# Optimization experiments

Hardware: AMD Instinct MI355X
Metric: run time of the kernel (lower is better)

The kernel has to match this reference:

```python
import jax, jax.numpy as jnp
import numpy as np

D_MODEL = 1024
N_HEADS = 16
HEAD_DIM = 64  # 16*64 = 1024
LATENT = 256   # low-rank KV compression dim
NUM_WHEELS = 4
WHEEL_OUT = 256


def setup_inputs() -> dict:
    key = jax.random.key(0)
    ks = jax.random.split(key, 9)
    S = 2048
    s = lambda fan_in: 1.0 / np.sqrt(fan_in)
    return {
        "sketch_emb": jax.random.normal(ks[0], (S, D_MODEL), dtype=jnp.float32),
        "Wq": jax.random.normal(ks[1], (D_MODEL, N_HEADS * HEAD_DIM), dtype=jnp.float32) * s(D_MODEL),
        "Wdkv": jax.random.normal(ks[2], (D_MODEL, LATENT), dtype=jnp.float32) * s(D_MODEL),
        "Wuk": jax.random.normal(ks[3], (LATENT, N_HEADS * HEAD_DIM), dtype=jnp.float32) * s(LATENT),
        "Wuv": jax.random.normal(ks[4], (LATENT, N_HEADS * HEAD_DIM), dtype=jnp.float32) * s(LATENT),
        "Wo": jax.random.normal(ks[5], (N_HEADS * HEAD_DIM, D_MODEL), dtype=jnp.float32) * s(N_HEADS * HEAD_DIM),
        "wheel_W": jax.random.normal(ks[6], (NUM_WHEELS, D_MODEL, WHEEL_OUT), dtype=jnp.float32) * s(D_MODEL),
        "wheel_b": jax.random.normal(ks[7], (NUM_WHEELS, WHEEL_OUT), dtype=jnp.float32) * 0.01,
    }


def reference(sketch_emb, Wq, Wdkv, Wuk, Wuv, Wo, wheel_W, wheel_b):
    S = sketch_emb.shape[0]
    # Multi-head latent attention: per-head Q, shared low-rank KV latent.
    q = (sketch_emb @ Wq).reshape(S, N_HEADS, HEAD_DIM)          # [S,H,D]
    c_kv = sketch_emb @ Wdkv                                      # [S,L]
    k = (c_kv @ Wuk).reshape(S, N_HEADS, HEAD_DIM)                # [S,H,D]
    v = (c_kv @ Wuv).reshape(S, N_HEADS, HEAD_DIM)                # [S,H,D]
    scale = 1.0 / np.sqrt(HEAD_DIM).astype(np.float32)
    scores = jnp.einsum("qhd,khd->hqk", q, k) * scale             # [H,S,S]
    attn = jax.nn.softmax(scores, axis=-1)
    ctx = jnp.einsum("hqk,khd->qhd", attn, v).reshape(S, N_HEADS * HEAD_DIM)
    body = ctx @ Wo                                               # [S,1024]
    # Wheel projections batched as one einsum, then laid out as concat order
    # cat([body, w0, w1, w2, w3], dim=1)
    wheels = jnp.einsum("sd,wde->swe", body, wheel_W) + wheel_b   # [S,W,256]
    wheels = wheels.reshape(S, NUM_WHEELS * WHEEL_OUT)
    return jnp.concatenate([body, wheels], axis=1)                # [S,2048]
```

## Files before the change

kernel.cpp:

```cpp
#include <hip/hip_runtime.h>
#include <math.h>

#define S_LEN 2048
#define DMODEL 1024
#define NHEADS 16
#define HDIM 64
#define QPITCH 1280

typedef _Float16 f16x8 __attribute__((ext_vector_type(8)));
typedef _Float16 f16x4 __attribute__((ext_vector_type(4)));
typedef float    f32x4 __attribute__((ext_vector_type(4)));

__device__ __forceinline__ void gld_lds16(void* lds, const void* g) {
    __builtin_amdgcn_global_load_lds(
        (__attribute__((address_space(1))) void*)(g),
        (__attribute__((address_space(3))) void*)(lds), 16, 0, 0);
}

__device__ __forceinline__ void gemm_core(
    _Float16* sA, _Float16* sB,
    const _Float16* __restrict__ A, int lda,
    const _Float16* __restrict__ Bt, int ldb,
    int nkt,
    _Float16* __restrict__ Cb, int ldcb, int bmode,
    _Float16* __restrict__ Cb2, int ldcb2,
    int bx, int by)
{
    const int tid  = threadIdx.x;
    const int lane = tid & 63;
    const int w    = tid >> 6;
    const int quad = lane >> 4;
    const int c0   = lane & 15;
    const int m0 = by * 128;
    const int n0 = bx * 128;

    const int srow = lane >> 3;
    const int sc   = lane & 7;
    const _Float16* a_src[4]; const _Float16* b_src[4];
    int dstoff[4];
#pragma unroll
    for (int t = 0; t < 4; t++) {
        const int row = w * 32 + t * 8 + srow;
        const int c = sc ^ (row & 7);
        a_src[t] = A  + (size_t)(m0 + row) * lda + c * 8;
        b_src[t] = Bt + (size_t)(n0 + row) * ldb + c * 8;
        dstoff[t] = (w * 32 + t * 8) * 64;
    }

    const int mw = (w & 1) * 64;
    const int nw = (w >> 1) * 64;
    int arow[4], brow[4];
#pragma unroll
    for (int i = 0; i < 4; i++) {
        arow[i] = mw + i * 16 + c0;
        brow[i] = nw + i * 16 + c0;
    }

    f32x4 acc[4][4];
#pragma unroll
    for (int i = 0; i < 4; i++)
#pragma unroll
        for (int j = 0; j < 4; j++) acc[i][j] = (f32x4){0.f, 0.f, 0.f, 0.f};

    auto stage = [&](int buf) {
#pragma unroll
        for (int t = 0; t < 4; t++) {
            gld_lds16(&sA[buf * 8192 + dstoff[t]], a_src[t]); a_src[t] += 64;
            gld_lds16(&sB[buf * 8192 + dstoff[t]], b_src[t]); b_src[t] += 64;
        }
    };
    auto step = [&](int buf) {
#pragma unroll
        for (int ks = 0; ks < 2; ks++) {
            const int cb = ks * 4 + quad;
            f16x8 af[4], bfv[4];
#pragma unroll
            for (int i = 0; i < 4; i++)
                af[i] = *(const f16x8*)&sA[buf * 8192 + arow[i] * 64 + ((cb ^ (arow[i] & 7)) << 3)];
#pragma unroll
            for (int j = 0; j < 4; j++)
                bfv[j] = *(const f16x8*)&sB[buf * 8192 + brow[j] * 64 + ((cb ^ (brow[j] & 7)) << 3)];
#pragma unroll
            for (int i = 0; i < 4; i++)
#pragma unroll
                for (int j = 0; j < 4; j++)
                    acc[i][j] = __builtin_amdgcn_mfma_f32_16x16x32_f16(af[i], bfv[j], acc[i][j], 0, 0, 0);
        }
    };

    stage(0);
    for (int kt = 0; kt < nkt; kt += 2) {
        __syncthreads();
        stage(1);
        step(0);
        __syncthreads();
        if (kt + 2 < nkt) stage(0);
        step(1);
    }

#pragma unroll
    for (int i = 0; i < 4; i++) {
#pragma unroll
        for (int reg = 0; reg < 4; reg++) {
            const int m = m0 + mw + i * 16 + quad * 4 + reg;
#pragma unroll
            for (int j = 0; j < 4; j++) {
                const int n = n0 + nw + j * 16 + c0;
                _Float16 hv = (_Float16)acc[i][j][reg];
                if (bmode == 0) {
                    Cb[(size_t)m * ldcb + n] = hv;
                } else {
                    if (n < 1024) Cb[(size_t)m * ldcb + n] = hv;
                    else          Cb2[(size_t)(n - 1024) * ldcb2 + m] = hv;
                }
            }
        }
    }
}

__global__ __launch_bounds__(256) void gemm_qcwf(
    const _Float16* __restrict__ WcT, const _Float16* __restrict__ Wo_f16,
    _Float16* __restrict__ BtWheels,
    const _Float16* __restrict__ emb_f16, const _Float16* __restrict__ Wqc_t,
    _Float16* __restrict__ qc_f16)
{
    __shared__ _Float16 sA[2][8192];
    __shared__ _Float16 sB[2][8192];
    int b = blockIdx.x;
    if (b < 64) {
        gemm_core(&sA[0][0], &sB[0][0], WcT, 1024, Wo_f16, 1024, 16,
                  BtWheels, 1024, 0, nullptr, 0, b >> 3, b & 7);
    } else {
        b -= 64;
        gemm_core(&sA[0][0], &sB[0][0], emb_f16, 1024, Wqc_t, 1024, 16,
                  qc_f16, 1280, 0, nullptr, 0, b >> 4, b & 15);
    }
}

__global__ __launch_bounds__(256) void gemm_kv(
    const _Float16* __restrict__ qc_f16, const _Float16* __restrict__ Wukv_t,
    _Float16* __restrict__ k_f16, _Float16* __restrict__ vT_f16)
{
    __shared__ _Float16 sA[2][8192];
    __shared__ _Float16 sB[2][8192];
    const int b = blockIdx.x;
    gemm_core(&sA[0][0], &sB[0][0], qc_f16 + 1024, 1280, Wukv_t, 256, 4,
              k_f16, 1024, 4, vT_f16, 2048, b >> 4, b & 15);
}

__global__ __launch_bounds__(256) void gemm_fin64(
    const _Float16* __restrict__ A,
    const _Float16* __restrict__ Bt,
    float* __restrict__ out,
    const float* __restrict__ bias)
{
    __shared__ _Float16 sA[2][64 * 64];
    __shared__ _Float16 sB[2][128 * 64];

    const int tid  = threadIdx.x;
    const int lane = tid & 63;
    const int w    = tid >> 6;
    const int quad = lane >> 4;
    const int c0   = lane & 15;

    const int flat = blockIdx.x;
    const int xcd  = flat & 7;
    const int wi   = flat >> 3;
    const int by   = (xcd & 3) * 8 + (wi & 7);
    const int bx   = (xcd >> 2) * 8 + (wi >> 3);
    const int m0 = by * 64;
    const int n0 = bx * 128;

    const int srow = lane >> 3;
    const int sc   = lane & 7;
    const _Float16* a_src[2]; int a_dst[2];
#pragma unroll
    for (int t = 0; t < 2; t++) {
        const int row = t * 32 + w * 8 + srow;
        const int c = sc ^ (row & 7);
        a_src[t] = A + (size_t)(m0 + row) * 1024 + c * 8;
        a_dst[t] = (t * 32 + w * 8) * 64;
    }
    const _Float16* b_src[4]; int b_dst[4];
#pragma unroll
    for (int t = 0; t < 4; t++) {
        const int row = t * 32 + w * 8 + srow;
        const int c = sc ^ (row & 7);
        b_src[t] = Bt + (size_t)(n0 + row) * 1024 + c * 8;
        b_dst[t] = (t * 32 + w * 8) * 64;
    }

    const int mw = (w & 1) * 32;
    const int nw = (w >> 1) * 64;
    int arow[2], brow[4];
#pragma unroll
    for (int i = 0; i < 2; i++) arow[i] = mw + i * 16 + c0;
#pragma unroll
    for (int j = 0; j < 4; j++) brow[j] = nw + j * 16 + c0;

    f32x4 acc[2][4];
#pragma unroll
    for (int i = 0; i < 2; i++)
#pragma unroll
        for (int j = 0; j < 4; j++) acc[i][j] = (f32x4){0.f, 0.f, 0.f, 0.f};

    auto stage = [&](int buf) {
#pragma unroll
        for (int t = 0; t < 2; t++) { gld_lds16(&sA[buf][a_dst[t]], a_src[t]); a_src[t] += 64; }
#pragma unroll
        for (int t = 0; t < 4; t++) { gld_lds16(&sB[buf][b_dst[t]], b_src[t]); b_src[t] += 64; }
    };
    auto step = [&](int buf) {
#pragma unroll
        for (int ks = 0; ks < 2; ks++) {
            const int cb = ks * 4 + quad;
            f16x8 af[2], bfv[4];
#pragma unroll
            for (int i = 0; i < 2; i++)
                af[i] = *(const f16x8*)&sA[buf][arow[i] * 64 + ((cb ^ (arow[i] & 7)) << 3)];
#pragma unroll
            for (int j = 0; j < 4; j++)
                bfv[j] = *(const f16x8*)&sB[buf][brow[j] * 64 + ((cb ^ (brow[j] & 7)) << 3)];
#pragma unroll
            for (int i = 0; i < 2; i++)
#pragma unroll
                for (int j = 0; j < 4; j++)
                    acc[i][j] = __builtin_amdgcn_mfma_f32_16x16x32_f16(af[i], bfv[j], acc[i][j], 0, 0, 0);
        }
    };

    stage(0);
    for (int kt = 0; kt < 16; kt += 2) {
        __syncthreads();
        stage(1);
        step(0);
        __syncthreads();
        if (kt + 2 < 16) stage(0);
        step(1);
    }

    float bias_v[4];
#pragma unroll
    for (int j = 0; j < 4; j++) bias_v[j] = bias[n0 + nw + j * 16 + c0];
#pragma unroll
    for (int i = 0; i < 2; i++) {
#pragma unroll
        for (int reg = 0; reg < 4; reg++) {
            const int m = m0 + mw + i * 16 + quad * 4 + reg;
#pragma unroll
            for (int j = 0; j < 4; j++) {
                const int n = n0 + nw + j * 16 + c0;
                out[(size_t)m * 2048 + n] = acc[i][j][reg] + bias_v[j];
            }
        }
    }
}

#define SOFT_M2 8.65617024533378f
#define OTP 68

__global__ __launch_bounds__(256) void attn_mfma_kernel(
    const _Float16* __restrict__ qs,
    const _Float16* __restrict__ kk,
    const _Float16* __restrict__ vT,
    float* __restrict__ Opart,
    float* __restrict__ lpart)
{
    __shared__ _Float16 Ks[2][64 * 64];
    __shared__ _Float16 Vt[2][64 * 64];
    __shared__ float    Ot[4][16 * OTP];

    const int flat = blockIdx.x;
    const int g  = flat & 31;
    const int qb = flat >> 5;
    const int h  = g & 15;
    const int kz = g >> 4;
    const int tid  = threadIdx.x;
    const int lane = tid & 63;
    const int w    = tid >> 6;
    const int quad = lane >> 4;
    const int c0   = lane & 15;

    f16x8 qfrag[2][2];
#pragma unroll
    for (int m = 0; m < 2; m++) {
        const _Float16* qrow = qs + (size_t)(qb * 128 + w * 32 + m * 16 + c0) * QPITCH + h * HDIM;
        qfrag[m][0] = *(const f16x8*)(qrow + quad * 8);
        qfrag[m][1] = *(const f16x8*)(qrow + 32 + quad * 8);
    }

    const int srow = lane >> 3;
    const int sc   = lane & 7;
    const _Float16* k_src[2]; const _Float16* v_src[2];
    int dstoff[2];
#pragma unroll
    for (int t = 0; t < 2; t++) {
        const int row = w * 16 + t * 8 + srow;
        const int c = sc ^ (row & 7);
        k_src[t] = kk + (size_t)(kz * 1024 + row) * DMODEL + h * HDIM + c * 8;
        v_src[t] = vT + (size_t)(h * HDIM + row) * S_LEN + kz * 1024 + c * 8;
        dstoff[t] = (w * 16 + t * 8) * 64;
    }

    f32x4 OfragT[2][4];
#pragma unroll
    for (int m = 0; m < 2; m++)
#pragma unroll
        for (int db = 0; db < 4; db++) OfragT[m][db] = (f32x4){0.f, 0.f, 0.f, 0.f};
    float l_r[2] = {0.f, 0.f};

    auto stage = [&](int buf) {
#pragma unroll
        for (int t = 0; t < 2; t++) {
            gld_lds16(&Ks[buf][dstoff[t]], k_src[t]); k_src[t] += (size_t)64 * DMODEL;
            gld_lds16(&Vt[buf][dstoff[t]], v_src[t]); v_src[t] += 64;
        }
    };

    auto attn_step = [&](int buf) {
        f32x4 sfrag[2][4];
#pragma unroll
        for (int m = 0; m < 2; m++)
#pragma unroll
            for (int nb = 0; nb < 4; nb++) sfrag[m][nb] = (f32x4){0.f, 0.f, 0.f, 0.f};
        __builtin_amdgcn_s_setprio(1);
#pragma unroll
        for (int nb = 0; nb < 4; nb++) {
            const int krow = nb * 16 + c0;
#pragma unroll
            for (int ks = 0; ks < 2; ks++) {
                const int cb = ks * 4 + quad;
                f16x8 kfr = *(const f16x8*)&Ks[buf][krow * 64 + ((cb ^ (c0 & 7)) << 3)];
#pragma unroll
                for (int m = 0; m < 2; m++)
                    sfrag[m][nb] = __builtin_amdgcn_mfma_f32_16x16x32_f16(kfr, qfrag[m][ks], sfrag[m][nb], 0, 0, 0);
            }
        }
        __builtin_amdgcn_s_setprio(0);

        f16x4 pfrag[2][4];
#pragma unroll
        for (int m = 0; m < 2; m++)
#pragma unroll
            for (int kb = 0; kb < 4; kb++) {
                float p0 = __builtin_amdgcn_exp2f(sfrag[m][kb][0] - SOFT_M2);
                float p1 = __builtin_amdgcn_exp2f(sfrag[m][kb][1] - SOFT_M2);
                float p2 = __builtin_amdgcn_exp2f(sfrag[m][kb][2] - SOFT_M2);
                float p3 = __builtin_amdgcn_exp2f(sfrag[m][kb][3] - SOFT_M2);
                l_r[m] += (p0 + p1) + (p2 + p3);
                f16x4 pv;
                pv[0] = (_Float16)p0; pv[1] = (_Float16)p1;
                pv[2] = (_Float16)p2; pv[3] = (_Float16)p3;
                pfrag[m][kb] = pv;
            }

        __builtin_amdgcn_s_setprio(1);
#pragma unroll
        for (int kb = 0; kb < 4; kb++) {
            const int cc = (((kb * 2 + (quad >> 1)) ^ (c0 & 7)) << 3) + (quad & 1) * 4;
#pragma unroll
            for (int db = 0; db < 4; db++) {
                f16x4 vf = *(const f16x4*)&Vt[buf][(db * 16 + c0) * 64 + cc];
#pragma unroll
                for (int m = 0; m < 2; m++)
                    OfragT[m][db] = __builtin_amdgcn_mfma_f32_16x16x16f16(vf, pfrag[m][kb], OfragT[m][db], 0, 0, 0);
            }
        }
        __builtin_amdgcn_s_setprio(0);
    };

    stage(0);
    for (int kt = 0; kt < 16; kt += 2) {
        __syncthreads();
        stage(1);
        attn_step(0);
        __syncthreads();
        if (kt + 2 < 16) stage(0);
        attn_step(1);
    }

#pragma unroll
    for (int m = 0; m < 2; m++) {
        float rs = l_r[m];
        rs += __shfl_xor(rs, 16, 64);
        rs += __shfl_xor(rs, 32, 64);
        if (lane < 16)
            lpart[(size_t)(kz * 16 + h) * 2048 + qb * 128 + w * 32 + m * 16 + c0] = rs;
    }

    float* Otw = &Ot[w][0];
#pragma unroll
    for (int m = 0; m < 2; m++) {
#pragma unroll
        for (int db = 0; db < 4; db++)
            *(f32x4*)&Otw[c0 * OTP + db * 16 + quad * 4] = OfragT[m][db];
        __asm__ __volatile__("s_waitcnt lgkmcnt(0)" ::: "memory");
#pragma unroll
        for (int it = 0; it < 4; it++) {
            const int r = it * 4 + quad;
            f32x4 ov = *(const f32x4*)&Otw[r * OTP + c0 * 4];
            const int row = qb * 128 + w * 32 + m * 16 + r;
            *(f32x4*)&Opart[((size_t)kz * 2048 + row) * 1024 + h * 64 + c0 * 4] = ov;
        }
        __asm__ __volatile__("s_waitcnt lgkmcnt(0)" ::: "memory");
    }
}

__global__ __launch_bounds__(256) void attn_combine_kernel(
    const float* __restrict__ Opart, const float* __restrict__ lpart,
    _Float16* __restrict__ ctx)
{
    const int i = blockIdx.x * 256 + threadIdx.x;
    const int row = i >> 8;
    const int c4  = (i & 255) * 4;
    const int h = c4 >> 6;
    const float l = lpart[(size_t)h * 2048 + row] + lpart[(size_t)(16 + h) * 2048 + row];
    const float inv = 1.0f / l;
    float4 o0 = ((const float4*)(Opart + (size_t)row * 1024))[c4 >> 2];
    float4 o1 = ((const float4*)(Opart + (size_t)(2048 + row) * 1024))[c4 >> 2];
    f16x4 v;
    v[0] = (_Float16)((o0.x + o1.x) * inv);
    v[1] = (_Float16)((o0.y + o1.y) * inv);
    v[2] = (_Float16)((o0.z + o1.z) * inv);
    v[3] = (_Float16)((o0.w + o1.w) * inv);
    *(f16x4*)(ctx + (size_t)row * 1024 + c4) = v;
}

__device__ __forceinline__ void xpose_seg(float (*tile)[33],
    const float* __restrict__ src, _Float16* __restrict__ dst,
    int C, int dpitch, float scale, int bx, int by, int nbase0)
{
    const int r0 = by * 32, c0 = bx * 32;
    const int tr = threadIdx.x >> 5, tc = threadIdx.x & 31;
#pragma unroll
    for (int i = 0; i < 4; i++)
        tile[tr + i * 8][tc] = src[(size_t)(r0 + tr + i * 8) * C + c0 + tc];
    __syncthreads();
    const int nr = threadIdx.x & 31;
    const int k0 = (threadIdx.x >> 5) * 4;
    f16x4 hv;
#pragma unroll
    for (int e = 0; e < 4; e++)
        hv[e] = (_Float16)(tile[k0 + e][nr] * scale);
    *(f16x4*)(dst + (size_t)(nbase0 + c0 + nr) * dpitch + (r0 + k0)) = hv;
}

__global__ __launch_bounds__(256) void megaprep_kernel(
    const float* __restrict__ emb, const float* __restrict__ Wq,
    const float* __restrict__ Wdkv, const float* __restrict__ Wuk,
    const float* __restrict__ Wuv, const float* __restrict__ Wo,
    const float* __restrict__ wheelW, const float* __restrict__ wheelB,
    _Float16* __restrict__ Wqc_t, _Float16* __restrict__ Wukv_t,
    _Float16* __restrict__ Bt_full, _Float16* __restrict__ WcT,
    _Float16* __restrict__ Wo_f16, _Float16* __restrict__ emb_f16,
    float* __restrict__ biasbuf)
{
    __shared__ float tile[32][33];
    int b = blockIdx.x;
    const int tid = threadIdx.x;

    if (b < 1024) { xpose_seg(tile, Wq, Wqc_t, 1024, 1024, 0.125f, b & 31, b >> 5, 0); return; }
    b -= 1024;
    if (b < 256)  { xpose_seg(tile, Wdkv, Wqc_t + 1048576, 256, 1024, 1.f, b & 7, b >> 3, 0); return; }
    b -= 256;
    if (b < 256)  { xpose_seg(tile, Wuk, Wukv_t, 1024, 256, 1.4426950408889634f, b & 31, b >> 5, 0); return; }
    b -= 256;
    if (b < 256)  { xpose_seg(tile, Wuv, Wukv_t + 262144, 1024, 256, 1.f, b & 31, b >> 5, 0); return; }
    b -= 256;
    if (b < 1024) { xpose_seg(tile, Wo, Bt_full, 1024, 1024, 1.f, b & 31, b >> 5, 0); return; }
    b -= 1024;
    if (b < 1024) {
        const int z = b >> 8, rem = b & 255;
        xpose_seg(tile, wheelW + (size_t)z * 262144, WcT, 256, 1024, 1.f,
                  rem & 7, rem >> 3, z * 256);
        return;
    }
    b -= 1024;
    if (b < 1024) {
        const int i = b * 256 + tid;
        float4 f = ((const float4*)Wo)[i];
        f16x4 v;
        v[0] = (_Float16)f.x; v[1] = (_Float16)f.y;
        v[2] = (_Float16)f.z; v[3] = (_Float16)f.w;
        ((f16x4*)Wo_f16)[i] = v;
        return;
    }
    b -= 1024;
    if (b < 2048) {
        const int i = b * 256 + tid;
        float4 f = ((const float4*)emb)[i];
        f16x4 v;
        v[0] = (_Float16)f.x; v[1] = (_Float16)f.y;
        v[2] = (_Float16)f.z; v[3] = (_Float16)f.w;
        ((f16x4*)emb_f16)[i] = v;
        return;
    }
    b -= 2048;
    if (b < 8) {
        const int i = b * 256 + tid;
        biasbuf[i] = (i < 1024) ? 0.f : wheelB[i - 1024];
    }
}

extern "C" void kernel_launch(void* const* d_in, const int* in_sizes, int n_in,
                              void* d_out, int out_size, void* d_ws, size_t ws_size,
                              hipStream_t stream) {
    const float* emb    = (const float*)d_in[0];
    const float* Wq     = (const float*)d_in[1];
    const float* Wdkv   = (const float*)d_in[2];
    const float* Wuk    = (const float*)d_in[3];
    const float* Wuv    = (const float*)d_in[4];
    const float* Wo     = (const float*)d_in[5];
    const float* wheelW = (const float*)d_in[6];
    const float* wheelB = (const float*)d_in[7];
    float* out = (float*)d_out;

    _Float16* ws = (_Float16*)d_ws;
    _Float16* Bt_full = ws;
    _Float16* Wqc_t   = ws + 2097152;
    _Float16* Wukv_t  = ws + 3407872;
    float*    biasbuf = (float*)(ws + 3932160);
    _Float16* WcT     = ws + 3936256;
    _Float16* Wo_f16  = ws + 4984832;
    _Float16* ctx     = ws + 3936256;
    _Float16* emb_f16 = ws + 6033408;
    _Float16* qc_f16  = ws + 8130560;
    _Float16* k_f16   = ws + 10752000;
    _Float16* vT_f16  = ws + 12849152;
    float*    Opart   = (float*)(ws + 14946304);
    float*    lpart   = (float*)(ws + 23334912);

    megaprep_kernel<<<6920, 256, 0, stream>>>(
        emb, Wq, Wdkv, Wuk, Wuv, Wo, wheelW, wheelB,
        Wqc_t, Wukv_t, Bt_full, WcT, Wo_f16, emb_f16, biasbuf);

    gemm_qcwf<<<224, 256, 0, stream>>>(WcT, Wo_f16, Bt_full + (size_t)1024 * 1024,
                                       emb_f16, Wqc_t, qc_f16);

    gemm_kv<<<256, 256, 0, stream>>>(qc_f16, Wukv_t, k_f16, vT_f16);

    attn_mfma_kernel<<<512, 256, 0, stream>>>(qc_f16, k_f16, vT_f16, Opart, lpart);

    attn_combine_kernel<<<2048, 256, 0, stream>>>(Opart, lpart, ctx);

    gemm_fin64<<<512, 256, 0, stream>>>(ctx, Bt_full, out, biasbuf);
}
```

Before: 170.9 us.

## Triple-buffer LDS staging with counted vmcnt waits and single barrier per tile

The GEMM and attention kernels move from a double-buffered loop with two __syncthreads per pair of tiles to a three-stage ring buffer. Loads run two tiles ahead, and each iteration waits only on the older async global-to-LDS loads through explicit vmcnt counts, followed by one raw s_barrier. The aim is to hide more global load latency and cut barrier stalls. In exchange it uses 50% more LDS per block, which can lower occupancy, and correctness relies on the hand-picked vmcnt counts matching the number of loads issued per stage.

```diff
diff --git a/kernel.cpp b/kernel.cpp
--- a/kernel.cpp
+++ b/kernel.cpp
@@ -15,6 +15,16 @@
     __builtin_amdgcn_global_load_lds(
         (__attribute__((address_space(1))) void*)(g),
         (__attribute__((address_space(3))) void*)(lds), 16, 0, 0);
+}
+
+__device__ __forceinline__ void vm_wait0() { __asm__ __volatile__("s_waitcnt vmcnt(0)" ::: "memory"); }
+__device__ __forceinline__ void vm_wait4() { __asm__ __volatile__("s_waitcnt vmcnt(4)" ::: "memory"); }
+__device__ __forceinline__ void vm_wait6() { __asm__ __volatile__("s_waitcnt vmcnt(6)" ::: "memory"); }
+__device__ __forceinline__ void vm_wait8() { __asm__ __volatile__("s_waitcnt vmcnt(8)" ::: "memory"); }
+__device__ __forceinline__ void barrier_raw() {
+    __asm__ __volatile__("" ::: "memory");
+    __builtin_amdgcn_s_barrier();
+    __asm__ __volatile__("" ::: "memory");
 }
 
 __device__ __forceinline__ void gemm_core(
@@ -88,14 +98,14 @@
         }
     };
 
-    stage(0);
-    for (int kt = 0; kt < nkt; kt += 2) {
-        __syncthreads();
-        stage(1);
-        step(0);
-        __syncthreads();
-        if (kt + 2 < nkt) stage(0);
-        step(1);
+    stage(0); stage(1);
+    int cur = 0;
+    for (int kt = 0; kt < nkt; ++kt) {
+        if (kt < nkt - 1) vm_wait8(); else vm_wait0();
+        barrier_raw();
+        if (kt + 2 < nkt) { int nx = cur + 2; if (nx >= 3) nx -= 3; stage(nx); }
+        step(cur);
+        if (++cur == 3) cur = 0;
     }
 
 #pragma unroll
@@ -124,8 +134,8 @@
     const _Float16* __restrict__ emb_f16, const _Float16* __restrict__ Wqc_t,
     _Float16* __restrict__ qc_f16)
 {
-    __shared__ _Float16 sA[2][8192];
-    __shared__ _Float16 sB[2][8192];
+    __shared__ _Float16 sA[3][8192];
+    __shared__ _Float16 sB[3][8192];
     int b = blockIdx.x;
     if (b < 64) {
         gemm_core(&sA[0][0], &sB[0][0], WcT, 1024, Wo_f16, 1024, 16,
@@ -141,8 +151,8 @@
     const _Float16* __restrict__ qc_f16, const _Float16* __restrict__ Wukv_t,
     _Float16* __restrict__ k_f16, _Float16* __restrict__ vT_f16)
 {
-    __shared__ _Float16 sA[2][8192];
-    __shared__ _Float16 sB[2][8192];
+    __shared__ _Float16 sA[3][8192];
+    __shared__ _Float16 sB[3][8192];
     const int b = blockIdx.x;
     gemm_core(&sA[0][0], &sB[0][0], qc_f16 + 1024, 1280, Wukv_t, 256, 4,
               k_f16, 1024, 4, vT_f16, 2048, b >> 4, b & 15);
@@ -154,8 +164,8 @@
     float* __restrict__ out,
     const float* __restrict__ bias)
 {
-    __shared__ _Float16 sA[2][64 * 64];
-    __shared__ _Float16 sB[2][128 * 64];
+    __shared__ _Float16 sA[3][64 * 64];
+    __shared__ _Float16 sB[3][128 * 64];
 
     const int tid  = threadIdx.x;
     const int lane = tid & 63;
@@ -229,14 +239,14 @@
         }
     };
 
-    stage(0);
-    for (int kt = 0; kt < 16; kt += 2) {
-        __syncthreads();
-        stage(1);
-        step(0);
-        __syncthreads();
-        if (kt + 2 < 16) stage(0);
-        step(1);
+    stage(0); stage(1);
+    int cur = 0;
+    for (int kt = 0; kt < 16; ++kt) {
+        if (kt < 15) vm_wait6(); else vm_wait0();
+        barrier_raw();
+        if (kt + 2 < 16) { int nx = cur + 2; if (nx >= 3) nx -= 3; stage(nx); }
+        step(cur);
+        if (++cur == 3) cur = 0;
     }
 
     float bias_v[4];
@@ -266,8 +276,8 @@
     float* __restrict__ Opart,
     float* __restrict__ lpart)
 {
-    __shared__ _Float16 Ks[2][64 * 64];
-    __shared__ _Float16 Vt[2][64 * 64];
+    __shared__ _Float16 Ks[3][64 * 64];
+    __shared__ _Float16 Vt[3][64 * 64];
     __shared__ float    Ot[4][16 * OTP];
 
     const int flat = blockIdx.x;
@@ -369,14 +379,14 @@
         __builtin_amdgcn_s_setprio(0);
     };
 
-    stage(0);
-    for (int kt = 0; kt < 16; kt += 2) {
-        __syncthreads();
-        stage(1);
-        attn_step(0);
-        __syncthreads();
-        if (kt + 2 < 16) stage(0);
-        attn_step(1);
+    stage(0); stage(1);
+    int cur = 0;
+    for (int kt = 0; kt < 16; ++kt) {
+        if (kt < 15) vm_wait4(); else vm_wait0();
+        barrier_raw();
+        if (kt + 2 < 16) { int nx = cur + 2; if (nx >= 3) nx -= 3; stage(nx); }
+        attn_step(cur);
+        if (++cur == 3) cur = 0;
     }
 
 #pragma unroll
```

Result: no change. 168.0 us (-1.7%).
